# Kernel tuning notes

Hardware: AMD Instinct MI355X
Metric: run time of the kernel (lower is better)

The kernel has to match this reference:

```python
import math
import jax, jax.numpy as jnp
import numpy as np

B, NPC, K, D, T, L = 512, 32, 12, 64, 64, 4  # crystals, atoms/crystal, knn, node_dim, time_dim, layers
N = B * NPC
E_IN = 2 * D + 1 + T   # 193
N_IN = 2 * D + T       # 192


def setup_inputs() -> dict:
    key = jax.random.key(0)
    ks = jax.random.split(key, 32)
    rn = lambda k, shp, s=0.05: jax.random.normal(k, shp, jnp.float32) * s
    inp = {}
    inp["z_nodes"] = jax.random.normal(ks[0], (N, 128), jnp.float32)
    inp["t"] = jax.random.uniform(ks[1], (B,), jnp.float32) * 1000.0
    inp["frac_coords"] = jax.random.uniform(ks[2], (N, 3), jnp.float32)
    inp["lattice"] = jnp.eye(3, dtype=jnp.float32) * 5.0 + rn(ks[3], (B, 3, 3), 0.3)
    inp["batch_indices"] = jnp.repeat(jnp.arange(B, dtype=jnp.int32), NPC)
    inp["num_atoms"] = NPC
    # time_mlp: Linear(T, 2T) -> SiLU -> Linear(2T, T)
    inp["time_w1"] = rn(ks[4], (T, 2 * T)); inp["time_b1"] = rn(ks[5], (2 * T,))
    inp["time_w2"] = rn(ks[6], (2 * T, T)); inp["time_b2"] = rn(ks[7], (T,))
    # node_embedding: Linear(128, D)
    inp["emb_w"] = rn(ks[8], (128, D)); inp["emb_b"] = rn(ks[9], (D,))
    # per-layer EGNN params stacked on leading L axis
    inp["edge_w1"] = rn(ks[10], (L, E_IN, D)); inp["edge_b1"] = rn(ks[11], (L, D))
    inp["edge_w2"] = rn(ks[12], (L, D, D));    inp["edge_b2"] = rn(ks[13], (L, D))
    inp["coord_w1"] = rn(ks[14], (L, D, D));   inp["coord_b1"] = rn(ks[15], (L, D))
    inp["coord_w2"] = rn(ks[16], (L, D, 1))
    inp["node_w1"] = rn(ks[17], (L, N_IN, D)); inp["node_b1"] = rn(ks[18], (L, D))
    inp["node_w2"] = rn(ks[19], (L, D, D));    inp["node_b2"] = rn(ks[20], (L, D))
    return inp


def _forward(z_nodes, t, frac_coords, lattice, batch_indices, num_atoms,
             time_w1, time_b1, time_w2, time_b2, emb_w, emb_b,
             edge_w1, edge_b1, edge_w2, edge_b2, coord_w1, coord_b1, coord_w2,
             node_w1, node_b1, node_w2, node_b2):
    silu = jax.nn.silu
    n = num_atoms
    b = lattice.shape[0]
    n_nodes = z_nodes.shape[0]

    # ---- time embedding ----
    half = T // 2
    freqs = jnp.exp(jnp.arange(half, dtype=jnp.float32) * (-math.log(10000.0) / (half - 1)))
    ang = t[:, None] * freqs[None, :]
    sinu = jnp.concatenate([jnp.sin(ang), jnp.cos(ang)], axis=-1)  # [B, T]
    t_feat = silu(sinu @ time_w1 + time_b1) @ time_w2 + time_b2     # [B, T]
    t_nodes = t_feat[batch_indices]                                  # [N, T]

    h = z_nodes @ emb_w + emb_b                                      # [N, D]

    # ---- vectorized PBC KNN graph (all crystals have n atoms) ----
    f = frac_coords.reshape(b, n, 3)
    diff_f = f[:, :, None, :] - f[:, None, :, :]
    diff_f = diff_f - jnp.round(diff_f)
    diff_c = jnp.einsum('bijk,bkl->bijl', diff_f, lattice)           # [b,n,n,3]
    dist_sq = jnp.sum(diff_c * diff_c, axis=-1)                      # [b,n,n]
    dist_sq = jnp.where(jnp.eye(n, dtype=bool)[None], jnp.inf, dist_sq)
    k = min(K, n - 1)
    _, idx = jax.lax.top_k(-dist_sq, k)                              # [b,n,k] neighbor indices
    offs = (jnp.arange(b, dtype=jnp.int32) * n)[:, None, None]
    edge_src = (idx + offs).reshape(-1)                              # neighbors j
    edge_dst = (jnp.broadcast_to(jnp.arange(n, dtype=jnp.int32)[None, :, None], (b, n, k)) + offs).reshape(-1)
    diff_cart = jnp.take_along_axis(diff_c, jnp.broadcast_to(idx[..., None], (b, n, k, 3)), axis=2).reshape(-1, 3)
    dist_sq_e = jnp.take_along_axis(dist_sq, idx, axis=2).reshape(-1, 1)

    t_edges = t_nodes[edge_src]                                      # [E, T]

    total_shift = jnp.zeros((n_nodes, 3), dtype=h.dtype)
    for l in range(L):
        edge_in = jnp.concatenate([h[edge_src], h[edge_dst], dist_sq_e, t_edges], axis=-1)
        m = silu(edge_in @ edge_w1[l] + edge_b1[l])
        m = silu(m @ edge_w2[l] + edge_b2[l])                        # [E, D]
        cw = silu(m @ coord_w1[l] + coord_b1[l]) @ coord_w2[l]       # [E, 1]
        coord_update = jax.ops.segment_sum(diff_cart * cw, edge_src, num_segments=n_nodes)
        m_i = jax.ops.segment_sum(m, edge_dst, num_segments=n_nodes)
        node_in = jnp.concatenate([h, m_i, t_nodes], axis=-1)
        h = h + (silu(node_in @ node_w1[l] + node_b1[l]) @ node_w2[l] + node_b2[l])
        total_shift = total_shift + coord_update

    inv_lat = jnp.linalg.inv(lattice)[batch_indices]                 # [N,3,3]
    shift_frac = jnp.einsum('ni,nij->nj', total_shift, inv_lat)
    return shift_frac, h


def reference(z_nodes, t, frac_coords, lattice, batch_indices, num_atoms,
              time_w1, time_b1, time_w2, time_b2, emb_w, emb_b,
              edge_w1, edge_b1, edge_w2, edge_b2, coord_w1, coord_b1, coord_w2,
              node_w1, node_b1, node_w2, node_b2):
    return _forward(z_nodes, t, frac_coords, lattice, batch_indices, num_atoms,
                    time_w1, time_b1, time_w2, time_b2, emb_w, emb_b,
                    edge_w1, edge_b1, edge_w2, edge_b2, coord_w1, coord_b1, coord_w2,
                    node_w1, node_b1, node_w2, node_b2)
```

## Files before the change

### kernel.cpp

```cpp
#include <hip/hip_runtime.h>
#include <hip/hip_bf16.h>
#include <math.h>

#define NB 512
#define NPC 32
#define KNN 12
#define NL 4
#define NN (NB*NPC)
#define WPL 28672
#define TSTR 68

typedef float v4f __attribute__((ext_vector_type(4)));
typedef float v2f __attribute__((ext_vector_type(2)));
typedef short s8v __attribute__((ext_vector_type(8)));

__device__ __forceinline__ float silu_f(float x) {
    return x * __builtin_amdgcn_rcpf(1.0f + __builtin_amdgcn_exp2f(x * -1.44269504088896341f));
}

__device__ __forceinline__ v2f silu2(v2f x) {
    v2f n = x * -1.44269504088896341f;
    v2f e; e.x = __builtin_amdgcn_exp2f(n.x); e.y = __builtin_amdgcn_exp2f(n.y);
    v2f d = e + 1.0f;
    v2f r; r.x = __builtin_amdgcn_rcpf(d.x); r.y = __builtin_amdgcn_rcpf(d.y);
    return x * r;
}

__device__ __forceinline__ unsigned short f2bf(float x) {
    unsigned u = __float_as_uint(x);
    u += 0x7fffu + ((u >> 16) & 1u);
    return (unsigned short)(u >> 16);
}

__device__ __forceinline__ unsigned pk2bf(float a, float b) {
    __hip_bfloat162 t = __float22bfloat162_rn(make_float2(a, b));
    union { __hip_bfloat162 h; unsigned u; } c; c.h = t;
    return c.u;
}
__device__ __forceinline__ unsigned pk2bfu(v2f s) { return pk2bf(s.x, s.y); }

__device__ __forceinline__ int div12(int e) { return (e * 1366) >> 14; }

template<int R>
__device__ __forceinline__ void gemm_acc(const float* A, int astride,
                                         const float* __restrict__ Wg,
                                         int K, int lane, float* acc) {
#pragma unroll 2
    for (int kq = 0; kq < (K >> 2); ++kq) {
        float w0 = Wg[(4*kq+0)*64 + lane];
        float w1 = Wg[(4*kq+1)*64 + lane];
        float w2 = Wg[(4*kq+2)*64 + lane];
        float w3 = Wg[(4*kq+3)*64 + lane];
#pragma unroll
        for (int r = 0; r < R; ++r) {
            float4 a = *(const float4*)(A + r*astride + 4*kq);
            acc[r] = fmaf(a.x, w0, acc[r]);
            acc[r] = fmaf(a.y, w1, acc[r]);
            acc[r] = fmaf(a.z, w2, acc[r]);
            acc[r] = fmaf(a.w, w3, acc[r]);
        }
    }
}

extern "C" __global__ void prepack_w(const float* __restrict__ edge_w1, const float* __restrict__ edge_w2,
                                     const float* __restrict__ coord_w1, const float* __restrict__ node_w1,
                                     const float* __restrict__ node_w2, unsigned short* __restrict__ wout) {
    int g = blockIdx.x * 256 + threadIdx.x;
    if (g >= 4 * WPL / 8) return;
    int l = (g * 8) / WPL;
    int r = (g * 8) % WPL;
    int base, nKt, mat;
    if      (r < 8192)  { base = 0;     nKt = 2; mat = 0; }
    else if (r < 12288) { base = 8192;  nKt = 2; mat = 1; }
    else if (r < 16384) { base = 12288; nKt = 2; mat = 2; }
    else if (r < 24576) { base = 16384; nKt = 4; mat = 3; }
    else                { base = 24576; nKt = 2; mat = 4; }
    int idx = r - base;
    int lane = (idx >> 3) & 63, t = idx >> 9;
    int kt = t % nKt, nt = t / nKt;
    int k0 = kt*32 + ((lane >> 4) & 3)*8;
    int n  = nt*16 + (lane & 15);
    unsigned short o[8];
#pragma unroll
    for (int j = 0; j < 8; ++j) {
        int k = k0 + j;
        float v;
        if      (mat == 0) v = (n < 64) ? edge_w1[l*193*64 + k*64 + n] : edge_w1[l*193*64 + (64+k)*64 + (n-64)];
        else if (mat == 1) v = edge_w2 [l*4096 + k*64 + n];
        else if (mat == 2) v = coord_w1[l*4096 + k*64 + n];
        else if (mat == 3) v = node_w1 [l*192*64 + k*64 + n];
        else               v = node_w2 [l*4096 + k*64 + n];
        o[j] = f2bf(v);
    }
    *(s8v*)(wout + g*8) = *(s8v*)o;
}

extern "C" __global__ __launch_bounds__(512, 4)
void crystal_fused(const float* __restrict__ z_nodes, const float* __restrict__ t_in,
                   const float* __restrict__ frac,    const float* __restrict__ lattice,
                   const float* __restrict__ time_w1, const float* __restrict__ time_b1,
                   const float* __restrict__ time_w2, const float* __restrict__ time_b2,
                   const float* __restrict__ emb_w,   const float* __restrict__ emb_b,
                   const float* __restrict__ edge_w1, const float* __restrict__ edge_b1,
                   const float* __restrict__ edge_b2, const float* __restrict__ coord_b1,
                   const float* __restrict__ coord_w2,
                   const float* __restrict__ node_w1, const float* __restrict__ node_b1,
                   const float* __restrict__ node_b2,
                   const unsigned short* __restrict__ wbf,
                   float* __restrict__ out)
{
    __shared__ __align__(16) unsigned short s_habf[32*136];
    __shared__ __align__(16) float s_hs[32*68];
    __shared__ __align__(16) float s_hd[32*68];
    __shared__ __align__(16) unsigned short s_tiles16[8*16*TSTR];
    __shared__ __align__(16) unsigned short s_w2bf[4096];
    __shared__ __align__(16) unsigned short s_wc1bf[4096];
    __shared__ __align__(16) float s_w1r[64];
    __shared__ float s_edsq[384];
    __shared__ unsigned short s_esrc[384];
    __shared__ float s_endc[384*3];
    __shared__ float s_frac[32][3];
    __shared__ float s_lat[9], s_inv[9];
    __shared__ float s_sinu[64], s_t1[128], s_tf[64];
    __shared__ float s_tb4[NL*64], s_nb4[NL*64];
    __shared__ float s_shift[32*3];

    float* dcf = (float*)s_tiles16;
    float (*s_dsq)[33] = (float(*)[33])((char*)s_tiles16 + 12288);
    float* s_hf = (float*)s_tiles16;
    unsigned short* s_n1bf = s_tiles16;

    const int tid  = threadIdx.x;
    const int c    = blockIdx.x;
    const int lane = tid & 63;
    const int wave = tid >> 6;
    const int q4   = lane >> 4;
    const int c16  = lane & 15;
    const int base = c * NPC;

    if (tid < 96) {
        ((float*)s_frac)[tid] = frac[base*3 + tid];
    } else if (tid < 105) {
        s_lat[tid-96] = lattice[c*9 + (tid-96)];
    } else if (tid >= 128 && tid < 160) {
        int i = tid - 128;
        float freq = expf((float)i * (-9.210340371976184f / 31.0f));
        float ang  = t_in[c] * freq;
        s_sinu[i]    = sinf(ang);
        s_sinu[i+32] = cosf(ang);
    }
    __syncthreads();

    {
        float l00=s_lat[0],l01=s_lat[1],l02=s_lat[2];
        float l10=s_lat[3],l11=s_lat[4],l12=s_lat[5];
        float l20=s_lat[6],l21=s_lat[7],l22=s_lat[8];
        for (int p = tid; p < 1024; p += 512) {
            int i = p >> 5, j = p & 31;
            float dx = s_frac[i][0]-s_frac[j][0];
            float dy = s_frac[i][1]-s_frac[j][1];
            float dz = s_frac[i][2]-s_frac[j][2];
            dx -= rintf(dx); dy -= rintf(dy); dz -= rintf(dz);
            float cx = dx*l00 + dy*l10 + dz*l20;
            float cy = dx*l01 + dy*l11 + dz*l21;
            float cz = dx*l02 + dy*l12 + dz*l22;
            float dd = cx*cx + cy*cy + cz*cz;
            s_dsq[i][j] = (i==j) ? 3.0e38f : dd;
            dcf[p*3+0]=cx; dcf[p*3+1]=cy; dcf[p*3+2]=cz;
        }
    }
    __syncthreads();

    if (tid < 256) {
        int i = tid >> 3, g = tid & 7;
        float d0 = s_dsq[i][g*4+0];
        float d1 = s_dsq[i][g*4+1];
        float d2 = s_dsq[i][g*4+2];
        float d3 = s_dsq[i][g*4+3];
        for (int k = 0; k < KNN; ++k) {
            float v = d0; int jl = g*4;
            if (d1 < v) { v = d1; jl = g*4+1; }
            if (d2 < v) { v = d2; jl = g*4+2; }
            if (d3 < v) { v = d3; jl = g*4+3; }
            float ov; int oj;
            ov = __shfl_xor(v, 1); oj = __shfl_xor(jl, 1);
            if (ov < v || (ov == v && oj < jl)) { v = ov; jl = oj; }
            ov = __shfl_xor(v, 2); oj = __shfl_xor(jl, 2);
            if (ov < v || (ov == v && oj < jl)) { v = ov; jl = oj; }
            ov = __shfl_xor(v, 4); oj = __shfl_xor(jl, 4);
            if (ov < v || (ov == v && oj < jl)) { v = ov; jl = oj; }
            if ((jl >> 2) == g) {
                int s = jl & 3;
                if      (s == 0) d0 = 3.9e38f;
                else if (s == 1) d1 = 3.9e38f;
                else if (s == 2) d2 = 3.9e38f;
                else             d3 = 3.9e38f;
            }
            if (g == 0) {
                int e = i*KNN + k;
                s_edsq[e] = v;
                s_esrc[e] = (unsigned short)jl;
                int p = (i<<5) + jl;
                s_endc[e*3+0] = dcf[p*3+0];
                s_endc[e*3+1] = dcf[p*3+1];
                s_endc[e*3+2] = dcf[p*3+2];
            }
        }
    } else if (tid < 384) {
        int jj = tid - 256;
        float p0 = time_b1[jj], p1=0.f, p2=0.f, p3=0.f;
        for (int k = 0; k < 64; k += 4) {
            p0 = fmaf(s_sinu[k+0], time_w1[(k+0)*128+jj], p0);
            p1 = fmaf(s_sinu[k+1], time_w1[(k+1)*128+jj], p1);
            p2 = fmaf(s_sinu[k+2], time_w1[(k+2)*128+jj], p2);
            p3 = fmaf(s_sinu[k+3], time_w1[(k+3)*128+jj], p3);
        }
        s_t1[jj] = silu_f((p0+p1) + (p2+p3));
    }
    __syncthreads();

    if (tid < 64) {
        float p0=time_b2[tid],p1=0.f,p2=0.f,p3=0.f;
        for (int k = 0; k < 128; k += 4) {
            p0 = fmaf(s_t1[k+0], time_w2[(k+0)*64+tid], p0);
            p1 = fmaf(s_t1[k+1], time_w2[(k+1)*64+tid], p1);
            p2 = fmaf(s_t1[k+2], time_w2[(k+2)*64+tid], p2);
            p3 = fmaf(s_t1[k+3], time_w2[(k+3)*64+tid], p3);
        }
        s_tf[tid] = (p0+p1) + (p2+p3);
    } else if (tid < 160) {
        s_shift[tid-64] = 0.0f;
    }
    __syncthreads();

    {
        int lt = wave >> 1, kind = wave & 1;
        const float* Wt = kind ? (node_w1 + lt*192*64 + 128*64) : (edge_w1 + lt*193*64 + 129*64);
        const float* bb = kind ? (node_b1 + lt*64) : (edge_b1 + lt*64);
        float p0 = bb[lane], p1=0.f, p2=0.f, p3=0.f;
        for (int k = 0; k < 64; k += 4) {
            p0 = fmaf(s_tf[k+0], Wt[(k+0)*64 + lane], p0);
            p1 = fmaf(s_tf[k+1], Wt[(k+1)*64 + lane], p1);
            p2 = fmaf(s_tf[k+2], Wt[(k+2)*64 + lane], p2);
            p3 = fmaf(s_tf[k+3], Wt[(k+3)*64 + lane], p3);
        }
        float v = (p0+p1) + (p2+p3);
        if (kind) s_nb4[lt*64 + lane] = v;
        else      s_tb4[lt*64 + lane] = v;
    }
    {
        float acc[4];
#pragma unroll
        for (int r = 0; r < 4; ++r) acc[r] = emb_b[lane];
        gemm_acc<4>(z_nodes + (base + wave*4)*128, 128, emb_w, 128, lane, acc);
#pragma unroll
        for (int r = 0; r < 4; ++r) {
            int row = wave*4 + r;
            s_hf[row*64 + lane] = acc[r];
            s_habf[row*136 + lane] = f2bf(acc[r]);
        }
    }
    __syncthreads();

    const int mtA = wave & 1, ntA = wave >> 1;
    float h_reg[4];
    {
        int colh = ntA*16 + c16;
#pragma unroll
        for (int r = 0; r < 4; ++r)
            h_reg[r] = s_hf[(mtA*16 + q4*4 + r)*64 + colh];
    }

    for (int l = 0; l < NL; ++l) {
        const unsigned short* wl = wbf + l*WPL;

        *(s8v*)(s_w2bf  + tid*8) = *(const s8v*)(wl +  8192 + tid*8);
        *(s8v*)(s_wc1bf + tid*8) = *(const s8v*)(wl + 12288 + tid*8);
        if (tid < 64) s_w1r[tid] = edge_w1[l*193*64 + 128*64 + tid];

        float b2e_v[4], cb1_v[4], w2c_v[4];
#pragma unroll
        for (int nt = 0; nt < 4; ++nt) {
            b2e_v[nt] = edge_b2 [l*64 + nt*16 + c16];
            cb1_v[nt] = coord_b1[l*64 + nt*16 + c16];
            w2c_v[nt] = coord_w2[l*64 + nt*16 + c16];
        }

        {
            const int wn = wave & 3;
            s8v a[2][2];
#pragma unroll
            for (int mt = 0; mt < 2; ++mt)
#pragma unroll
                for (int kt = 0; kt < 2; ++kt)
                    a[mt][kt] = *(const s8v*)(s_habf + (mt*16 + c16)*136 + kt*32 + q4*8);
            v4f acc[2] = {{0.f,0.f,0.f,0.f},{0.f,0.f,0.f,0.f}};
#pragma unroll
            for (int kt = 0; kt < 2; ++kt) {
                s8v b = *(const s8v*)(wl + (((wn + (wave >= 4 ? 4 : 0))*2 + kt)*64 + lane)*8);
#pragma unroll
                for (int mt = 0; mt < 2; ++mt)
                    acc[mt] = __builtin_amdgcn_mfma_f32_16x16x32_bf16(a[mt][kt], b, acc[mt], 0, 0, 0);
            }
            int col = wn*16 + c16;
            if (wave >= 4) {
                float tbv = s_tb4[l*64 + col];
#pragma unroll
                for (int mt = 0; mt < 2; ++mt)
#pragma unroll
                    for (int reg = 0; reg < 4; ++reg)
                        s_hd[(mt*16 + q4*4 + reg)*68 + col] = acc[mt][reg] + tbv;
            } else {
#pragma unroll
                for (int mt = 0; mt < 2; ++mt)
#pragma unroll
                    for (int reg = 0; reg < 4; ++reg)
                        s_hs[(mt*16 + q4*4 + reg)*68 + col] = acc[mt][reg];
            }
        }
        __syncthreads();

        {
            unsigned short* tile = s_tiles16 + wave*16*TSTR;
            float miacc[4][2];
#pragma unroll
            for (int a2 = 0; a2 < 4; ++a2) { miacc[a2][0] = 0.f; miacc[a2][1] = 0.f; }

            auto flushd = [&](int d) {
                int s = d & 1;
#pragma unroll
                for (int nt = 0; nt < 4; ++nt) {
                    float v = miacc[nt][s];
                    v += __shfl_xor(v, 16);
                    v += __shfl_xor(v, 32);
                    s_habf[(wave*4 + d)*136 + 64 + nt*16 + c16] = f2bf(v);
                    miacc[nt][s] = 0.f;
                }
            };

#pragma unroll 1
            for (int m = 0; m < 3; ++m) {
                const int e0g = wave*48 + m*16;
                const float dq = s_edsq[e0g + c16];
                const int srcn = s_esrc[e0g + c16];
                const int dstn = div12(e0g + c16);
                const float* hsr = s_hs + srcn*68;
                const float* hdr = s_hd + dstn*68;
                union S8 { s8v v; unsigned u[4]; } A0, A1;
#pragma unroll
                for (int g2 = 0; g2 < 4; ++g2) {
                    int off = ((g2 & 2) ? 32 : 0) + ((g2 & 1) ? 4 : 0) + q4*8;
                    float4 Hv = *(const float4*)(hsr + off);
                    float4 Gv = *(const float4*)(hdr + off);
                    float4 Wv = *(const float4*)(s_w1r + off);
                    v2f t0 = {Hv.x + Gv.x + Wv.x*dq, Hv.y + Gv.y + Wv.y*dq};
                    v2f t1 = {Hv.z + Gv.z + Wv.z*dq, Hv.w + Gv.w + Wv.w*dq};
                    unsigned lo  = pk2bfu(silu2(t0));
                    unsigned hi2 = pk2bfu(silu2(t1));
                    if (g2 < 2) { A0.u[g2*2] = lo; A0.u[g2*2+1] = hi2; }
                    else        { A1.u[(g2-2)*2] = lo; A1.u[(g2-2)*2+1] = hi2; }
                }

                const int thr = 3 - m;
                const int slo = m & 1;
#pragma unroll
                for (int nt = 0; nt < 4; ++nt) {
                    s8v b0 = *(const s8v*)(s_w2bf + ((nt*2+0)*64 + lane)*8);
                    s8v b1 = *(const s8v*)(s_w2bf + ((nt*2+1)*64 + lane)*8);
                    v4f acc = {0.f,0.f,0.f,0.f};
                    acc = __builtin_amdgcn_mfma_f32_16x16x32_bf16(A0.v, b0, acc, 0,0,0);
                    acc = __builtin_amdgcn_mfma_f32_16x16x32_bf16(A1.v, b1, acc, 0,0,0);
                    int col = nt*16 + c16;
                    v2f z01 = {acc[0] + b2e_v[nt], acc[1] + b2e_v[nt]};
                    v2f z23 = {acc[2] + b2e_v[nt], acc[3] + b2e_v[nt]};
                    v2f s01 = silu2(z01), s23 = silu2(z23);
                    unsigned p01 = pk2bfu(s01), p23 = pk2bfu(s23);
                    tile[(q4*4 + 0)*TSTR + col] = (unsigned short)p01;
                    tile[(q4*4 + 1)*TSTR + col] = (unsigned short)(p01 >> 16);
                    tile[(q4*4 + 2)*TSTR + col] = (unsigned short)p23;
                    tile[(q4*4 + 3)*TSTR + col] = (unsigned short)(p23 >> 16);
                    float msum = (s01.x + s01.y) + (s23.x + s23.y);
                    bool hi = (q4 >= thr);
                    miacc[nt][slo]     += hi ? 0.f : msum;
                    miacc[nt][slo ^ 1] += hi ? msum : 0.f;
                }
                asm volatile("s_waitcnt lgkmcnt(0)" ::: "memory");
                s8v c0 = *(const s8v*)(tile + c16*TSTR +      q4*8);
                s8v c1 = *(const s8v*)(tile + c16*TSTR + 32 + q4*8);
                v2f cwp01 = {0.f, 0.f}, cwp23 = {0.f, 0.f};
#pragma unroll
                for (int nt = 0; nt < 4; ++nt) {
                    s8v wb0 = *(const s8v*)(s_wc1bf + ((nt*2+0)*64 + lane)*8);
                    s8v wb1 = *(const s8v*)(s_wc1bf + ((nt*2+1)*64 + lane)*8);
                    v4f acc = {0.f,0.f,0.f,0.f};
                    acc = __builtin_amdgcn_mfma_f32_16x16x32_bf16(c0, wb0, acc, 0,0,0);
                    acc = __builtin_amdgcn_mfma_f32_16x16x32_bf16(c1, wb1, acc, 0,0,0);
                    v2f z01 = {acc[0] + cb1_v[nt], acc[1] + cb1_v[nt]};
                    v2f z23 = {acc[2] + cb1_v[nt], acc[3] + cb1_v[nt]};
                    cwp01 += silu2(z01) * w2c_v[nt];
                    cwp23 += silu2(z23) * w2c_v[nt];
                }
                float cwp[4] = {cwp01.x, cwp01.y, cwp23.x, cwp23.y};
#pragma unroll
                for (int reg = 0; reg < 4; ++reg) {
                    float v = cwp[reg];
                    v += __shfl_xor(v, 1); v += __shfl_xor(v, 2);
                    v += __shfl_xor(v, 4); v += __shfl_xor(v, 8);
                    int e = e0g + q4*4 + reg;
                    if (c16 < 3) {
                        int src = s_esrc[e];
                        atomicAdd(&s_shift[src*3 + c16], s_endc[e*3 + c16] * v);
                    }
                }
                if (m == 0)      { flushd(0); }
                else if (m == 1) { flushd(1); }
                else             { flushd(2); flushd(3); }
            }
        }

        s8v bn1[4];
#pragma unroll
        for (int kt = 0; kt < 4; ++kt)
            bn1[kt] = *(const s8v*)(wl + 16384 + ((ntA*4+kt)*64 + lane)*8);
        __syncthreads();

        {
            s8v aA[4];
#pragma unroll
            for (int kt = 0; kt < 4; ++kt)
                aA[kt] = *(const s8v*)(s_habf + (mtA*16 + c16)*136 + kt*32 + q4*8);
            int col = ntA*16 + c16;
            float nbc = s_nb4[l*64 + col];
            v4f acc = {0.f,0.f,0.f,0.f};
#pragma unroll
            for (int kt = 0; kt < 4; ++kt)
                acc = __builtin_amdgcn_mfma_f32_16x16x32_bf16(aA[kt], bn1[kt], acc, 0,0,0);
            v2f z01 = {acc[0] + nbc, acc[1] + nbc};
            v2f z23 = {acc[2] + nbc, acc[3] + nbc};
            unsigned p01 = pk2bfu(silu2(z01)), p23 = pk2bfu(silu2(z23));
            int r0 = mtA*16 + q4*4;
            s_n1bf[(r0+0)*72 + col] = (unsigned short)p01;
            s_n1bf[(r0+1)*72 + col] = (unsigned short)(p01 >> 16);
            s_n1bf[(r0+2)*72 + col] = (unsigned short)p23;
            s_n1bf[(r0+3)*72 + col] = (unsigned short)(p23 >> 16);
        }
        s8v bn2[2];
        bn2[0] = *(const s8v*)(wl + 24576 + ((ntA*2+0)*64 + lane)*8);
        bn2[1] = *(const s8v*)(wl + 24576 + ((ntA*2+1)*64 + lane)*8);
        __syncthreads();

        {
            s8v a0 = *(const s8v*)(s_n1bf + (mtA*16 + c16)*72 +      q4*8);
            s8v a1 = *(const s8v*)(s_n1bf + (mtA*16 + c16)*72 + 32 + q4*8);
            int col = ntA*16 + c16;
            float nb2_v = node_b2[l*64 + col];
            v4f acc = {0.f,0.f,0.f,0.f};
            acc = __builtin_amdgcn_mfma_f32_16x16x32_bf16(a0, bn2[0], acc, 0,0,0);
            acc = __builtin_amdgcn_mfma_f32_16x16x32_bf16(a1, bn2[1], acc, 0,0,0);
#pragma unroll
            for (int reg = 0; reg < 4; ++reg) {
                int row = mtA*16 + q4*4 + reg;
                float hn = h_reg[reg] + acc[reg] + nb2_v;
                h_reg[reg] = hn;
                if (l < NL-1) s_habf[row*136 + col] = f2bf(hn);
                else          out[NN*3 + base*64 + row*64 + col] = hn;
            }
        }
        __syncthreads();
    }

    if (tid == 0) {
        float a=s_lat[0],b=s_lat[1],cc=s_lat[2];
        float d=s_lat[3],e=s_lat[4],f =s_lat[5];
        float g=s_lat[6],h2=s_lat[7],i2=s_lat[8];
        float A  =  (e*i2 - f*h2);
        float Bm = -(d*i2 - f*g);
        float C  =  (d*h2 - e*g);
        float det = a*A + b*Bm + cc*C;
        float rd = 1.0f/det;
        s_inv[0] = A*rd;
        s_inv[1] = -(b*i2 - cc*h2)*rd;
        s_inv[2] =  (b*f  - cc*e )*rd;
        s_inv[3] = Bm*rd;
        s_inv[4] =  (a*i2 - cc*g )*rd;
        s_inv[5] = -(a*f  - cc*d )*rd;
        s_inv[6] = C*rd;
        s_inv[7] = -(a*h2 - b*g  )*rd;
        s_inv[8] =  (a*e  - b*d  )*rd;
    }
    __syncthreads();
    if (tid < 96) {
        int r = tid/3, j = tid%3;
        float v = s_shift[r*3+0]*s_inv[0*3+j]
                + s_shift[r*3+1]*s_inv[1*3+j]
                + s_shift[r*3+2]*s_inv[2*3+j];
        out[(base + r)*3 + j] = v;
    }
}

extern "C" void kernel_launch(void* const* d_in, const int* in_sizes, int n_in,
                              void* d_out, int out_size, void* d_ws, size_t ws_size,
                              hipStream_t stream) {
    unsigned short* wbf = (unsigned short*)d_ws;
    prepack_w<<<(4*WPL/8 + 255)/256, 256, 0, stream>>>(
        (const float*)d_in[12], (const float*)d_in[14], (const float*)d_in[16],
        (const float*)d_in[19], (const float*)d_in[21], wbf);
    crystal_fused<<<NB, 512, 0, stream>>>(
        (const float*)d_in[0],  (const float*)d_in[1],  (const float*)d_in[2],  (const float*)d_in[3],
        (const float*)d_in[6],  (const float*)d_in[7],  (const float*)d_in[8],  (const float*)d_in[9],
        (const float*)d_in[10], (const float*)d_in[11],
        (const float*)d_in[12], (const float*)d_in[13], (const float*)d_in[15],
        (const float*)d_in[17], (const float*)d_in[18],
        (const float*)d_in[19], (const float*)d_in[20], (const float*)d_in[22],
        wbf, (float*)d_out);
}
```

Measured before the change: 211.8 us.

## Use 1024-thread blocks with one destination node per edge tile, drop LDS weight staging

Doubles the block to 16 waves and reassigns the edge-MLP work so each wave handles two destination nodes, padding each node's 12 edges to a 16-row MFMA tile. This removes the div12 mapping and cross-node flush logic for message sums. The per-layer LDS copies of the edge_w2 and coord_w1 bf16 tiles are removed and fragments are read straight from global/L2, and LDS buffers are aliased to fit the larger tile area. The trade-offs are 25% wasted MFMA rows, more global weight traffic, idle waves during the node-MLP phases, and a register budget tightened by launch_bounds(1024,2).

```diff
diff --git a/kernel.cpp b/kernel.cpp
--- a/kernel.cpp
+++ b/kernel.cpp
@@ -8,7 +8,7 @@
 #define NL 4
 #define NN (NB*NPC)
 #define WPL 28672
-#define TSTR 68
+#define TSTR 72
 
 typedef float v4f __attribute__((ext_vector_type(4)));
 typedef float v2f __attribute__((ext_vector_type(2)));
@@ -38,8 +38,6 @@
     return c.u;
 }
 __device__ __forceinline__ unsigned pk2bfu(v2f s) { return pk2bf(s.x, s.y); }
-
-__device__ __forceinline__ int div12(int e) { return (e * 1366) >> 14; }
 
 template<int R>
 __device__ __forceinline__ void gemm_acc(const float* A, int astride,
@@ -95,7 +93,7 @@
     *(s8v*)(wout + g*8) = *(s8v*)o;
 }
 
-extern "C" __global__ __launch_bounds__(512, 4)
+extern "C" __global__ __launch_bounds__(1024, 2)
 void crystal_fused(const float* __restrict__ z_nodes, const float* __restrict__ t_in,
                    const float* __restrict__ frac,    const float* __restrict__ lattice,
                    const float* __restrict__ time_w1, const float* __restrict__ time_b1,
@@ -109,26 +107,26 @@
                    const unsigned short* __restrict__ wbf,
                    float* __restrict__ out)
 {
+    __shared__ __align__(16) unsigned short s_tiles16[16*16*TSTR];
     __shared__ __align__(16) unsigned short s_habf[32*136];
     __shared__ __align__(16) float s_hs[32*68];
     __shared__ __align__(16) float s_hd[32*68];
-    __shared__ __align__(16) unsigned short s_tiles16[8*16*TSTR];
-    __shared__ __align__(16) unsigned short s_w2bf[4096];
-    __shared__ __align__(16) unsigned short s_wc1bf[4096];
-    __shared__ __align__(16) float s_w1r[64];
+    __shared__ __align__(16) float s_endc[384*3];
     __shared__ float s_edsq[384];
     __shared__ unsigned short s_esrc[384];
-    __shared__ float s_endc[384*3];
-    __shared__ float s_frac[32][3];
+    __shared__ float s_shift[96];
     __shared__ float s_lat[9], s_inv[9];
-    __shared__ float s_sinu[64], s_t1[128], s_tf[64];
     __shared__ float s_tb4[NL*64], s_nb4[NL*64];
-    __shared__ float s_shift[32*3];
+    __shared__ float s_w1r[64];
 
     float* dcf = (float*)s_tiles16;
     float (*s_dsq)[33] = (float(*)[33])((char*)s_tiles16 + 12288);
-    float* s_hf = (float*)s_tiles16;
+    float* s_sinu = (float*)((char*)s_tiles16 + 16512);
+    float* s_t1   = (float*)((char*)s_tiles16 + 16768);
+    float* s_tf   = (float*)((char*)s_tiles16 + 17280);
+    float* s_hf   = (float*)s_tiles16;
     unsigned short* s_n1bf = s_tiles16;
+    float (*s_frac)[3] = (float(*)[3])s_shift;
 
     const int tid  = threadIdx.x;
     const int c    = blockIdx.x;
@@ -155,19 +153,18 @@
         float l00=s_lat[0],l01=s_lat[1],l02=s_lat[2];
         float l10=s_lat[3],l11=s_lat[4],l12=s_lat[5];
         float l20=s_lat[6],l21=s_lat[7],l22=s_lat[8];
-        for (int p = tid; p < 1024; p += 512) {
-            int i = p >> 5, j = p & 31;
-            float dx = s_frac[i][0]-s_frac[j][0];
-            float dy = s_frac[i][1]-s_frac[j][1];
-            float dz = s_frac[i][2]-s_frac[j][2];
-            dx -= rintf(dx); dy -= rintf(dy); dz -= rintf(dz);
-            float cx = dx*l00 + dy*l10 + dz*l20;
-            float cy = dx*l01 + dy*l11 + dz*l21;
-            float cz = dx*l02 + dy*l12 + dz*l22;
-            float dd = cx*cx + cy*cy + cz*cz;
-            s_dsq[i][j] = (i==j) ? 3.0e38f : dd;
-            dcf[p*3+0]=cx; dcf[p*3+1]=cy; dcf[p*3+2]=cz;
-        }
+        int p = tid;
+        int i = p >> 5, j = p & 31;
+        float dx = s_frac[i][0]-s_frac[j][0];
+        float dy = s_frac[i][1]-s_frac[j][1];
+        float dz = s_frac[i][2]-s_frac[j][2];
+        dx -= rintf(dx); dy -= rintf(dy); dz -= rintf(dz);
+        float cx = dx*l00 + dy*l10 + dz*l20;
+        float cy = dx*l01 + dy*l11 + dz*l21;
+        float cz = dx*l02 + dy*l12 + dz*l22;
+        float dd = cx*cx + cy*cy + cz*cz;
+        s_dsq[i][j] = (i==j) ? 3.0e38f : dd;
+        dcf[p*3+0]=cx; dcf[p*3+1]=cy; dcf[p*3+2]=cz;
     }
     __syncthreads();
 
@@ -233,7 +230,7 @@
     }
     __syncthreads();
 
-    {
+    if (wave < 8) {
         int lt = wave >> 1, kind = wave & 1;
         const float* Wt = kind ? (node_w1 + lt*192*64 + 128*64) : (edge_w1 + lt*193*64 + 129*64);
         const float* bb = kind ? (node_b1 + lt*64) : (edge_b1 + lt*64);
@@ -249,13 +246,13 @@
         else      s_tb4[lt*64 + lane] = v;
     }
     {
-        float acc[4];
-#pragma unroll
-        for (int r = 0; r < 4; ++r) acc[r] = emb_b[lane];
-        gemm_acc<4>(z_nodes + (base + wave*4)*128, 128, emb_w, 128, lane, acc);
-#pragma unroll
-        for (int r = 0; r < 4; ++r) {
-            int row = wave*4 + r;
+        float acc[2];
+#pragma unroll
+        for (int r = 0; r < 2; ++r) acc[r] = emb_b[lane];
+        gemm_acc<2>(z_nodes + (base + wave*2)*128, 128, emb_w, 128, lane, acc);
+#pragma unroll
+        for (int r = 0; r < 2; ++r) {
+            int row = wave*2 + r;
             s_hf[row*64 + lane] = acc[r];
             s_habf[row*136 + lane] = f2bf(acc[r]);
         }
@@ -263,8 +260,8 @@
     __syncthreads();
 
     const int mtA = wave & 1, ntA = wave >> 1;
-    float h_reg[4];
-    {
+    float h_reg[4] = {0.f, 0.f, 0.f, 0.f};
+    if (wave < 8) {
         int colh = ntA*16 + c16;
 #pragma unroll
         for (int r = 0; r < 4; ++r)
@@ -274,8 +271,6 @@
     for (int l = 0; l < NL; ++l) {
         const unsigned short* wl = wbf + l*WPL;
 
-        *(s8v*)(s_w2bf  + tid*8) = *(const s8v*)(wl +  8192 + tid*8);
-        *(s8v*)(s_wc1bf + tid*8) = *(const s8v*)(wl + 12288 + tid*8);
         if (tid < 64) s_w1r[tid] = edge_w1[l*193*64 + 128*64 + tid];
 
         float b2e_v[4], cb1_v[4], w2c_v[4];
@@ -288,64 +283,43 @@
 
         {
             const int wn = wave & 3;
-            s8v a[2][2];
-#pragma unroll
-            for (int mt = 0; mt < 2; ++mt)
-#pragma unroll
-                for (int kt = 0; kt < 2; ++kt)
-                    a[mt][kt] = *(const s8v*)(s_habf + (mt*16 + c16)*136 + kt*32 + q4*8);
-            v4f acc[2] = {{0.f,0.f,0.f,0.f},{0.f,0.f,0.f,0.f}};
+            const int mt = (wave >> 2) & 1;
+            const int sd = wave >> 3;
+            s8v a[2];
+#pragma unroll
+            for (int kt = 0; kt < 2; ++kt)
+                a[kt] = *(const s8v*)(s_habf + (mt*16 + c16)*136 + kt*32 + q4*8);
+            v4f acc = {0.f,0.f,0.f,0.f};
 #pragma unroll
             for (int kt = 0; kt < 2; ++kt) {
-                s8v b = *(const s8v*)(wl + (((wn + (wave >= 4 ? 4 : 0))*2 + kt)*64 + lane)*8);
-#pragma unroll
-                for (int mt = 0; mt < 2; ++mt)
-                    acc[mt] = __builtin_amdgcn_mfma_f32_16x16x32_bf16(a[mt][kt], b, acc[mt], 0, 0, 0);
+                s8v b = *(const s8v*)(wl + (((wn + sd*4)*2 + kt)*64 + lane)*8);
+                acc = __builtin_amdgcn_mfma_f32_16x16x32_bf16(a[kt], b, acc, 0, 0, 0);
             }
             int col = wn*16 + c16;
-            if (wave >= 4) {
+            if (sd) {
                 float tbv = s_tb4[l*64 + col];
 #pragma unroll
-                for (int mt = 0; mt < 2; ++mt)
-#pragma unroll
-                    for (int reg = 0; reg < 4; ++reg)
-                        s_hd[(mt*16 + q4*4 + reg)*68 + col] = acc[mt][reg] + tbv;
+                for (int reg = 0; reg < 4; ++reg)
+                    s_hd[(mt*16 + q4*4 + reg)*68 + col] = acc[reg] + tbv;
             } else {
 #pragma unroll
-                for (int mt = 0; mt < 2; ++mt)
-#pragma unroll
-                    for (int reg = 0; reg < 4; ++reg)
-                        s_hs[(mt*16 + q4*4 + reg)*68 + col] = acc[mt][reg];
+                for (int reg = 0; reg < 4; ++reg)
+                    s_hs[(mt*16 + q4*4 + reg)*68 + col] = acc[reg];
             }
         }
         __syncthreads();
 
         {
             unsigned short* tile = s_tiles16 + wave*16*TSTR;
-            float miacc[4][2];
-#pragma unroll
-            for (int a2 = 0; a2 < 4; ++a2) { miacc[a2][0] = 0.f; miacc[a2][1] = 0.f; }
-
-            auto flushd = [&](int d) {
-                int s = d & 1;
-#pragma unroll
-                for (int nt = 0; nt < 4; ++nt) {
-                    float v = miacc[nt][s];
-                    v += __shfl_xor(v, 16);
-                    v += __shfl_xor(v, 32);
-                    s_habf[(wave*4 + d)*136 + 64 + nt*16 + c16] = f2bf(v);
-                    miacc[nt][s] = 0.f;
-                }
-            };
-
 #pragma unroll 1
-            for (int m = 0; m < 3; ++m) {
-                const int e0g = wave*48 + m*16;
-                const float dq = s_edsq[e0g + c16];
-                const int srcn = s_esrc[e0g + c16];
-                const int dstn = div12(e0g + c16);
+            for (int t = 0; t < 2; ++t) {
+                const int d  = wave*2 + t;
+                const int e0 = d*KNN;
+                const int cc = (c16 < 12) ? c16 : 11;
+                const float dq = s_edsq[e0 + cc];
+                const int  srcn = s_esrc[e0 + cc];
                 const float* hsr = s_hs + srcn*68;
-                const float* hdr = s_hd + dstn*68;
+                const float* hdr = s_hd + d*68;
                 union S8 { s8v v; unsigned u[4]; } A0, A1;
 #pragma unroll
                 for (int g2 = 0; g2 < 4; ++g2) {
@@ -361,12 +335,11 @@
                     else        { A1.u[(g2-2)*2] = lo; A1.u[(g2-2)*2+1] = hi2; }
                 }
 
-                const int thr = 3 - m;
-                const int slo = m & 1;
+                float miacc[4] = {0.f, 0.f, 0.f, 0.f};
 #pragma unroll
                 for (int nt = 0; nt < 4; ++nt) {
-                    s8v b0 = *(const s8v*)(s_w2bf + ((nt*2+0)*64 + lane)*8);
-                    s8v b1 = *(const s8v*)(s_w2bf + ((nt*2+1)*64 + lane)*8);
+                    s8v b0 = *(const s8v*)(wl +  8192 + ((nt*2+0)*64 + lane)*8);
+                    s8v b1 = *(const s8v*)(wl +  8192 + ((nt*2+1)*64 + lane)*8);
                     v4f acc = {0.f,0.f,0.f,0.f};
                     acc = __builtin_amdgcn_mfma_f32_16x16x32_bf16(A0.v, b0, acc, 0,0,0);
                     acc = __builtin_amdgcn_mfma_f32_16x16x32_bf16(A1.v, b1, acc, 0,0,0);
@@ -379,10 +352,8 @@
                     tile[(q4*4 + 1)*TSTR + col] = (unsigned short)(p01 >> 16);
                     tile[(q4*4 + 2)*TSTR + col] = (unsigned short)p23;
                     tile[(q4*4 + 3)*TSTR + col] = (unsigned short)(p23 >> 16);
-                    float msum = (s01.x + s01.y) + (s23.x + s23.y);
-                    bool hi = (q4 >= thr);
-                    miacc[nt][slo]     += hi ? 0.f : msum;
-                    miacc[nt][slo ^ 1] += hi ? msum : 0.f;
+                    float msum = (q4 == 3) ? 0.f : ((s01.x + s01.y) + (s23.x + s23.y));
+                    miacc[nt] += msum;
                 }
                 asm volatile("s_waitcnt lgkmcnt(0)" ::: "memory");
                 s8v c0 = *(const s8v*)(tile + c16*TSTR +      q4*8);
@@ -390,8 +361,8 @@
                 v2f cwp01 = {0.f, 0.f}, cwp23 = {0.f, 0.f};
 #pragma unroll
                 for (int nt = 0; nt < 4; ++nt) {
-                    s8v wb0 = *(const s8v*)(s_wc1bf + ((nt*2+0)*64 + lane)*8);
-                    s8v wb1 = *(const s8v*)(s_wc1bf + ((nt*2+1)*64 + lane)*8);
+                    s8v wb0 = *(const s8v*)(wl + 12288 + ((nt*2+0)*64 + lane)*8);
+                    s8v wb1 = *(const s8v*)(wl + 12288 + ((nt*2+1)*64 + lane)*8);
                     v4f acc = {0.f,0.f,0.f,0.f};
                     acc = __builtin_amdgcn_mfma_f32_16x16x32_bf16(c0, wb0, acc, 0,0,0);
                     acc = __builtin_amdgcn_mfma_f32_16x16x32_bf16(c1, wb1, acc, 0,0,0);
@@ -406,25 +377,32 @@
                     float v = cwp[reg];
                     v += __shfl_xor(v, 1); v += __shfl_xor(v, 2);
                     v += __shfl_xor(v, 4); v += __shfl_xor(v, 8);
-                    int e = e0g + q4*4 + reg;
-                    if (c16 < 3) {
+                    int er = q4*4 + reg;
+                    if (c16 < 3 && er < 12) {
+                        int e = e0 + er;
                         int src = s_esrc[e];
                         atomicAdd(&s_shift[src*3 + c16], s_endc[e*3 + c16] * v);
                     }
                 }
-                if (m == 0)      { flushd(0); }
-                else if (m == 1) { flushd(1); }
-                else             { flushd(2); flushd(3); }
+#pragma unroll
+                for (int nt = 0; nt < 4; ++nt) {
+                    float v = miacc[nt];
+                    v += __shfl_xor(v, 16);
+                    v += __shfl_xor(v, 32);
+                    s_habf[d*136 + 64 + nt*16 + c16] = f2bf(v);
+                }
             }
         }
 
         s8v bn1[4];
-#pragma unroll
-        for (int kt = 0; kt < 4; ++kt)
-            bn1[kt] = *(const s8v*)(wl + 16384 + ((ntA*4+kt)*64 + lane)*8);
+        if (wave < 8) {
+#pragma unroll
+            for (int kt = 0; kt < 4; ++kt)
+                bn1[kt] = *(const s8v*)(wl + 16384 + ((ntA*4+kt)*64 + lane)*8);
+        }
         __syncthreads();
 
-        {
+        if (wave < 8) {
             s8v aA[4];
 #pragma unroll
             for (int kt = 0; kt < 4; ++kt)
@@ -445,11 +423,13 @@
             s_n1bf[(r0+3)*72 + col] = (unsigned short)(p23 >> 16);
         }
         s8v bn2[2];
-        bn2[0] = *(const s8v*)(wl + 24576 + ((ntA*2+0)*64 + lane)*8);
-        bn2[1] = *(const s8v*)(wl + 24576 + ((ntA*2+1)*64 + lane)*8);
+        if (wave < 8) {
+            bn2[0] = *(const s8v*)(wl + 24576 + ((ntA*2+0)*64 + lane)*8);
+            bn2[1] = *(const s8v*)(wl + 24576 + ((ntA*2+1)*64 + lane)*8);
+        }
         __syncthreads();
 
-        {
+        if (wave < 8) {
             s8v a0 = *(const s8v*)(s_n1bf + (mtA*16 + c16)*72 +      q4*8);
             s8v a1 = *(const s8v*)(s_n1bf + (mtA*16 + c16)*72 + 32 + q4*8);
             int col = ntA*16 + c16;
@@ -505,7 +485,7 @@
     prepack_w<<<(4*WPL/8 + 255)/256, 256, 0, stream>>>(
         (const float*)d_in[12], (const float*)d_in[14], (const float*)d_in[16],
         (const float*)d_in[19], (const float*)d_in[21], wbf);
-    crystal_fused<<<NB, 512, 0, stream>>>(
+    crystal_fused<<<NB, 1024, 0, stream>>>(
         (const float*)d_in[0],  (const float*)d_in[1],  (const float*)d_in[2],  (const float*)d_in[3],
         (const float*)d_in[6],  (const float*)d_in[7],  (const float*)d_in[8],  (const float*)d_in[9],
         (const float*)d_in[10], (const float*)d_in[11],
```

After: 285.3 us. 1.35x slower.
